# Kernel optimization log

Measured on AMD Instinct MI355X. Metric: run time of the kernel, lower is better.

## Reference

```python
import jax, jax.numpy as jnp
import numpy as np

N, D, F = 8192, 256, 64

def setup_inputs() -> dict:
    key = jax.random.key(0)
    ks = jax.random.split(key, 7)
    s = 0.02
    return {
        "x":  jax.random.normal(ks[0], (N, D), dtype=jnp.float32),
        "Wk": jax.random.normal(ks[1], (F, D), dtype=jnp.float32) * s,
        "bk": jax.random.normal(ks[2], (F,), dtype=jnp.float32) * s,
        "Wv": jax.random.normal(ks[3], (F, D), dtype=jnp.float32) * s,
        "bv": jax.random.normal(ks[4], (F,), dtype=jnp.float32) * s,
        "Wq": jax.random.normal(ks[5], (N, F, D), dtype=jnp.float32) * s,
        "bq": jax.random.normal(ks[6], (N, F), dtype=jnp.float32) * s,
    }

def reference(x, Wk, bk, Wv, bv, Wq, bq):
    # Shared K/V projections: (N, D) -> (N, F)
    k = x @ Wk.T + bk
    v = x @ Wv.T + bv
    # Per-node Q: node i uses its own weight Wq[i] on its own row x[i]
    q = jnp.einsum("nd,nfd->nf", x, Wq) + bq  # (N, F)
    # Scaled dot-product attention over nodes
    scale = 1.0 / jnp.sqrt(jnp.asarray(F, dtype=x.dtype))
    scores = (q @ k.T) * scale               # (N, N)
    attn = jax.nn.softmax(scores, axis=-1)
    return attn @ v                           # (N, F)
```

## Files before the change

### kernel.cpp

```cpp
#include <hip/hip_runtime.h>
#include <math.h>

#define NN 8192
#define DD 256
#define FF 64

typedef __attribute__((ext_vector_type(8))) __bf16 bf16x8;
typedef __attribute__((ext_vector_type(4))) __bf16 bf16x4;
typedef __attribute__((ext_vector_type(4))) float f32x4;

static __device__ __forceinline__ f32x4 mfma16(bf16x8 a, bf16x8 b, f32x4 c) {
    return __builtin_amdgcn_mfma_f32_16x16x32_bf16(a, b, c, 0, 0, 0);
}

__global__ __launch_bounds__(256) void proj_kernel(
    const float* __restrict__ x, const float* __restrict__ Wk,
    const float* __restrict__ bk, const float* __restrict__ Wv,
    const float* __restrict__ bv, const float* __restrict__ Wq,
    const float* __restrict__ bq,
    __bf16* __restrict__ q_bf, __bf16* __restrict__ k_bf,
    __bf16* __restrict__ vT)
{
    const int i = blockIdx.x;
    const int t = threadIdx.x;
    const int l = t & 63;
    const int w = t >> 6;

    const float4 xf = reinterpret_cast<const float4*>(x)[(size_t)i * 64 + l];

    const float4* wq4 = reinterpret_cast<const float4*>(Wq) + (size_t)i * 4096;
    const float4* wk4 = reinterpret_cast<const float4*>(Wk);
    const float4* wv4 = reinterpret_cast<const float4*>(Wv);

#pragma unroll
    for (int ff = 0; ff < 16; ++ff) {
        const int f = w * 16 + ff;
        float4 a = wq4[f * 64 + l];
        float s = a.x * xf.x + a.y * xf.y + a.z * xf.z + a.w * xf.w;
        s += __shfl_xor(s, 32, 64); s += __shfl_xor(s, 16, 64);
        s += __shfl_xor(s, 8, 64);  s += __shfl_xor(s, 4, 64);
        s += __shfl_xor(s, 2, 64);  s += __shfl_xor(s, 1, 64);
        if (l == 0) q_bf[(size_t)i * FF + f] = (__bf16)(s + bq[(size_t)i * FF + f]);
    }
#pragma unroll
    for (int ff = 0; ff < 16; ++ff) {
        const int f = w * 16 + ff;
        float4 a = wk4[f * 64 + l];
        float s = a.x * xf.x + a.y * xf.y + a.z * xf.z + a.w * xf.w;
        s += __shfl_xor(s, 32, 64); s += __shfl_xor(s, 16, 64);
        s += __shfl_xor(s, 8, 64);  s += __shfl_xor(s, 4, 64);
        s += __shfl_xor(s, 2, 64);  s += __shfl_xor(s, 1, 64);
        if (l == 0) k_bf[(size_t)i * FF + f] = (__bf16)(s + bk[f]);
    }
#pragma unroll
    for (int ff = 0; ff < 16; ++ff) {
        const int f = w * 16 + ff;
        float4 a = wv4[f * 64 + l];
        float s = a.x * xf.x + a.y * xf.y + a.z * xf.z + a.w * xf.w;
        s += __shfl_xor(s, 32, 64); s += __shfl_xor(s, 16, 64);
        s += __shfl_xor(s, 8, 64);  s += __shfl_xor(s, 4, 64);
        s += __shfl_xor(s, 2, 64);  s += __shfl_xor(s, 1, 64);
        if (l == 0) vT[(size_t)f * NN + i] = (__bf16)(s + bv[f]);
    }
}

__global__ __launch_bounds__(256) void attn_kernel(
    const __bf16* __restrict__ q_bf, const __bf16* __restrict__ k_bf,
    const __bf16* __restrict__ vT,
    float* __restrict__ Om, float* __restrict__ m_arr, float* __restrict__ l_arr,
    int kv_per_split)
{
    __shared__ __bf16 pT[4][16][64];

    const int lane = threadIdx.x & 63;
    const int wave = threadIdx.x >> 6;
    const int g = lane >> 4;
    const int qc = lane & 15;
    const int qb = blockIdx.x;
    const int s  = blockIdx.y;
    const int q0 = qb * 64 + wave * 16;
    const int qrow = q0 + qc;
    const float scale = 0.125f;
    const int sw = qc & 7;

    const bf16x8 qf0 = *reinterpret_cast<const bf16x8*>(q_bf + (size_t)qrow * FF + g * 8);
    const bf16x8 qf1 = *reinterpret_cast<const bf16x8*>(q_bf + (size_t)qrow * FF + 32 + g * 8);

    f32x4 o[4];
#pragma unroll
    for (int m = 0; m < 4; ++m) o[m] = (f32x4){0.f, 0.f, 0.f, 0.f};
    float mrun = -INFINITY;
    float lrun = 0.f;

    const int kv0 = s * kv_per_split;

    for (int kb = kv0; kb < kv0 + kv_per_split; kb += 64) {
        f32x4 sc[4];
#pragma unroll
        for (int kt = 0; kt < 4; ++kt) {
            const __bf16* kp = k_bf + (size_t)(kb + kt * 16 + qc) * FF + g * 8;
            bf16x8 a0 = *reinterpret_cast<const bf16x8*>(kp);
            bf16x8 a1 = *reinterpret_cast<const bf16x8*>(kp + 32);
            f32x4 acc = (f32x4){0.f, 0.f, 0.f, 0.f};
            acc = mfma16(a0, qf0, acc);
            acc = mfma16(a1, qf1, acc);
            sc[kt] = acc;
        }

        float mt = sc[0].x;
#pragma unroll
        for (int kt = 0; kt < 4; ++kt) {
            mt = fmaxf(mt, sc[kt].x); mt = fmaxf(mt, sc[kt].y);
            mt = fmaxf(mt, sc[kt].z); mt = fmaxf(mt, sc[kt].w);
        }
        mt = fmaxf(mt, __shfl_xor(mt, 16, 64));
        mt = fmaxf(mt, __shfl_xor(mt, 32, 64));
        const float mnew = fmaxf(mrun, mt * scale);
        const float alpha = __expf(mrun - mnew);

        float psum = 0.f;
#pragma unroll
        for (int kt = 0; kt < 4; ++kt) {
            float p0 = __expf(sc[kt].x * scale - mnew);
            float p1 = __expf(sc[kt].y * scale - mnew);
            float p2 = __expf(sc[kt].z * scale - mnew);
            float p3 = __expf(sc[kt].w * scale - mnew);
            psum += (p0 + p1) + (p2 + p3);
            bf16x4 pv;
            pv[0] = (__bf16)p0; pv[1] = (__bf16)p1;
            pv[2] = (__bf16)p2; pv[3] = (__bf16)p3;
            const int b = kt * 2 + (g >> 1);
            *reinterpret_cast<bf16x4*>(&pT[wave][qc][((b ^ sw) << 3) + (g & 1) * 4]) = pv;
        }
        psum += __shfl_xor(psum, 16, 64);
        psum += __shfl_xor(psum, 32, 64);
        lrun = lrun * alpha + psum;
        mrun = mnew;
#pragma unroll
        for (int m = 0; m < 4; ++m) o[m] *= alpha;

#pragma unroll
        for (int kk = 0; kk < 2; ++kk) {
            const int br = kk * 4 + g;
            bf16x8 pb = *reinterpret_cast<const bf16x8*>(&pT[wave][qc][(br ^ sw) << 3]);
            const __bf16* vp = vT + (size_t)qc * NN + kb + kk * 32 + g * 8;
#pragma unroll
            for (int m = 0; m < 4; ++m) {
                bf16x8 a = *reinterpret_cast<const bf16x8*>(vp + (size_t)m * 16 * NN);
                o[m] = mfma16(a, pb, o[m]);
            }
        }
    }

    float* op = Om + (size_t)s * FF * NN;
#pragma unroll
    for (int m = 0; m < 4; ++m) {
        op[(size_t)(m * 16 + g * 4 + 0) * NN + q0 + qc] = o[m].x;
        op[(size_t)(m * 16 + g * 4 + 1) * NN + q0 + qc] = o[m].y;
        op[(size_t)(m * 16 + g * 4 + 2) * NN + q0 + qc] = o[m].z;
        op[(size_t)(m * 16 + g * 4 + 3) * NN + q0 + qc] = o[m].w;
    }
    if (g == 0) {
        m_arr[s * NN + qrow] = mrun;
        l_arr[s * NN + qrow] = lrun;
    }
}

__global__ __launch_bounds__(256) void combine_kernel(
    const float* __restrict__ Om, const float* __restrict__ m_arr,
    const float* __restrict__ l_arr, float* __restrict__ out, int nsplit)
{
    const int idx = blockIdx.x * 256 + threadIdx.x;
    const int f = idx >> 13;
    const int i = idx & (NN - 1);

    float M = -INFINITY;
    for (int s = 0; s < nsplit; ++s) M = fmaxf(M, m_arr[s * NN + i]);
    float L = 0.f, acc = 0.f;
    for (int s = 0; s < nsplit; ++s) {
        float wgt = __expf(m_arr[s * NN + i] - M);
        L   += wgt * l_arr[s * NN + i];
        acc += wgt * Om[((size_t)s * FF + f) * NN + i];
    }
    out[(size_t)i * FF + f] = acc / L;
}

extern "C" void kernel_launch(void* const* d_in, const int* in_sizes, int n_in,
                              void* d_out, int out_size, void* d_ws, size_t ws_size,
                              hipStream_t stream) {
    const float* x  = (const float*)d_in[0];
    const float* Wk = (const float*)d_in[1];
    const float* bk = (const float*)d_in[2];
    const float* Wv = (const float*)d_in[3];
    const float* bv = (const float*)d_in[4];
    const float* Wq = (const float*)d_in[5];
    const float* bq = (const float*)d_in[6];
    float* out = (float*)d_out;

    const int nsplit = (ws_size >= (size_t)20447232) ? 8 : 4;
    const int kv_per_split = NN / nsplit;

    char* ws = (char*)d_ws;
    __bf16* q_bf = (__bf16*)(ws);
    __bf16* k_bf = (__bf16*)(ws + ((size_t)1 << 20));
    __bf16* vT   = (__bf16*)(ws + ((size_t)2 << 20));
    float*  Om   = (float*)(ws + ((size_t)3 << 20));
    float*  m_a  = (float*)(ws + ((size_t)3 << 20) + (size_t)nsplit * FF * NN * 4);
    float*  l_a  = (float*)((char*)m_a + (size_t)nsplit * NN * 4);

    hipLaunchKernelGGL(proj_kernel, dim3(NN), dim3(256), 0, stream,
                       x, Wk, bk, Wv, bv, Wq, bq, q_bf, k_bf, vT);
    hipLaunchKernelGGL(attn_kernel, dim3(NN / 64, nsplit), dim3(256), 0, stream,
                       q_bf, k_bf, vT, Om, m_a, l_a, kv_per_split);
    hipLaunchKernelGGL(combine_kernel, dim3(NN * FF / 256), dim3(256), 0, stream,
                       Om, m_a, l_a, out, nsplit);
}
```

Measured before the change: 894.7 us.

## Split projections, use MFMA for K/V, stage K/V tiles in LDS, fold scale into exp2

The single projection kernel becomes two. One computes Q with a shared-memory transpose reduction in place of per-output shuffle chains. The other computes K/V with bf16 MFMA tiles instead of scalar dot products. The attention kernel stages each 64-row K and V tile cooperatively into swizzled LDS shared by the four waves, replacing redundant per-wave global loads, and adds two barriers per iteration. The softmax scale and log2(e) are folded into Q so the kernel can use exp2 directly. K/V inputs are now rounded to bf16 before the MFMA, which lowers precision, and the workspace threshold for using 8 splits is raised.

```diff
diff --git a/kernel.cpp b/kernel.cpp
--- a/kernel.cpp
+++ b/kernel.cpp
@@ -5,6 +5,8 @@
 #define DD 256
 #define FF 64
 
+#define QSC (0.125f * 1.4426950408889634f)
+
 typedef __attribute__((ext_vector_type(8))) __bf16 bf16x8;
 typedef __attribute__((ext_vector_type(4))) __bf16 bf16x4;
 typedef __attribute__((ext_vector_type(4))) float f32x4;
@@ -13,54 +15,97 @@
     return __builtin_amdgcn_mfma_f32_16x16x32_bf16(a, b, c, 0, 0, 0);
 }
 
-__global__ __launch_bounds__(256) void proj_kernel(
-    const float* __restrict__ x, const float* __restrict__ Wk,
-    const float* __restrict__ bk, const float* __restrict__ Wv,
-    const float* __restrict__ bv, const float* __restrict__ Wq,
-    const float* __restrict__ bq,
-    __bf16* __restrict__ q_bf, __bf16* __restrict__ k_bf,
-    __bf16* __restrict__ vT)
-{
+__global__ __launch_bounds__(256) void proj_q_kernel(
+    const float* __restrict__ x, const float* __restrict__ Wq,
+    const float* __restrict__ bq, __bf16* __restrict__ q_bf)
+{
+    __shared__ float T[4][64 * 17];
+
     const int i = blockIdx.x;
-    const int t = threadIdx.x;
-    const int l = t & 63;
-    const int w = t >> 6;
+    const int l = threadIdx.x & 63;
+    const int w = threadIdx.x >> 6;
 
     const float4 xf = reinterpret_cast<const float4*>(x)[(size_t)i * 64 + l];
-
     const float4* wq4 = reinterpret_cast<const float4*>(Wq) + (size_t)i * 4096;
-    const float4* wk4 = reinterpret_cast<const float4*>(Wk);
-    const float4* wv4 = reinterpret_cast<const float4*>(Wv);
-
+
+    float pf[16];
 #pragma unroll
     for (int ff = 0; ff < 16; ++ff) {
         const int f = w * 16 + ff;
         float4 a = wq4[f * 64 + l];
-        float s = a.x * xf.x + a.y * xf.y + a.z * xf.z + a.w * xf.w;
-        s += __shfl_xor(s, 32, 64); s += __shfl_xor(s, 16, 64);
-        s += __shfl_xor(s, 8, 64);  s += __shfl_xor(s, 4, 64);
-        s += __shfl_xor(s, 2, 64);  s += __shfl_xor(s, 1, 64);
-        if (l == 0) q_bf[(size_t)i * FF + f] = (__bf16)(s + bq[(size_t)i * FF + f]);
-    }
-#pragma unroll
-    for (int ff = 0; ff < 16; ++ff) {
-        const int f = w * 16 + ff;
-        float4 a = wk4[f * 64 + l];
-        float s = a.x * xf.x + a.y * xf.y + a.z * xf.z + a.w * xf.w;
-        s += __shfl_xor(s, 32, 64); s += __shfl_xor(s, 16, 64);
-        s += __shfl_xor(s, 8, 64);  s += __shfl_xor(s, 4, 64);
-        s += __shfl_xor(s, 2, 64);  s += __shfl_xor(s, 1, 64);
-        if (l == 0) k_bf[(size_t)i * FF + f] = (__bf16)(s + bk[f]);
-    }
-#pragma unroll
-    for (int ff = 0; ff < 16; ++ff) {
-        const int f = w * 16 + ff;
-        float4 a = wv4[f * 64 + l];
-        float s = a.x * xf.x + a.y * xf.y + a.z * xf.z + a.w * xf.w;
-        s += __shfl_xor(s, 32, 64); s += __shfl_xor(s, 16, 64);
-        s += __shfl_xor(s, 8, 64);  s += __shfl_xor(s, 4, 64);
-        s += __shfl_xor(s, 2, 64);  s += __shfl_xor(s, 1, 64);
-        if (l == 0) vT[(size_t)f * NN + i] = (__bf16)(s + bv[f]);
+        pf[ff] = a.x * xf.x + a.y * xf.y + a.z * xf.z + a.w * xf.w;
+    }
+#pragma unroll
+    for (int ff = 0; ff < 16; ++ff) T[w][l * 17 + ff] = pf[ff];
+    const int f = l & 15;
+    const int c = l >> 4;
+    float s = 0.f;
+#pragma unroll
+    for (int j = 0; j < 16; ++j) s += T[w][(c * 16 + j) * 17 + f];
+    s += __shfl_xor(s, 16, 64);
+    s += __shfl_xor(s, 32, 64);
+    if (l < 16)
+        q_bf[(size_t)i * FF + w * 16 + l] =
+            (__bf16)((s + bq[(size_t)i * FF + w * 16 + l]) * QSC);
+}
+
+__global__ __launch_bounds__(256) void proj_kv_kernel(
+    const float* __restrict__ x, const float* __restrict__ Wk,
+    const float* __restrict__ bk, const float* __restrict__ Wv,
+    const float* __restrict__ bv,
+    __bf16* __restrict__ k_bf, __bf16* __restrict__ vT)
+{
+    const int lane = threadIdx.x & 63;
+    const int wave = threadIdx.x >> 6;
+    const int g = lane >> 4;
+    const int qc = lane & 15;
+    const int i0 = blockIdx.x * 64 + wave * 16;
+
+    f32x4 ack[4], acv[4];
+#pragma unroll
+    for (int nt = 0; nt < 4; ++nt) {
+        ack[nt] = (f32x4){0.f, 0.f, 0.f, 0.f};
+        acv[nt] = (f32x4){0.f, 0.f, 0.f, 0.f};
+    }
+
+    const float4* x4 = reinterpret_cast<const float4*>(x);
+#pragma unroll
+    for (int ks = 0; ks < 8; ++ks) {
+        float4 xa = x4[(size_t)(i0 + qc) * 64 + ks * 8 + g * 2];
+        float4 xb = x4[(size_t)(i0 + qc) * 64 + ks * 8 + g * 2 + 1];
+        bf16x8 af;
+        af[0] = (__bf16)xa.x; af[1] = (__bf16)xa.y; af[2] = (__bf16)xa.z; af[3] = (__bf16)xa.w;
+        af[4] = (__bf16)xb.x; af[5] = (__bf16)xb.y; af[6] = (__bf16)xb.z; af[7] = (__bf16)xb.w;
+#pragma unroll
+        for (int nt = 0; nt < 4; ++nt) {
+            const float* wkp = Wk + (size_t)(nt * 16 + qc) * DD + ks * 32 + g * 8;
+            const float* wvp = Wv + (size_t)(nt * 16 + qc) * DD + ks * 32 + g * 8;
+            float4 wa = reinterpret_cast<const float4*>(wkp)[0];
+            float4 wb = reinterpret_cast<const float4*>(wkp)[1];
+            bf16x8 bk8;
+            bk8[0] = (__bf16)wa.x; bk8[1] = (__bf16)wa.y; bk8[2] = (__bf16)wa.z; bk8[3] = (__bf16)wa.w;
+            bk8[4] = (__bf16)wb.x; bk8[5] = (__bf16)wb.y; bk8[6] = (__bf16)wb.z; bk8[7] = (__bf16)wb.w;
+            ack[nt] = mfma16(af, bk8, ack[nt]);
+            float4 va = reinterpret_cast<const float4*>(wvp)[0];
+            float4 vb = reinterpret_cast<const float4*>(wvp)[1];
+            bf16x8 bv8;
+            bv8[0] = (__bf16)va.x; bv8[1] = (__bf16)va.y; bv8[2] = (__bf16)va.z; bv8[3] = (__bf16)va.w;
+            bv8[4] = (__bf16)vb.x; bv8[5] = (__bf16)vb.y; bv8[6] = (__bf16)vb.z; bv8[7] = (__bf16)vb.w;
+            acv[nt] = mfma16(af, bv8, acv[nt]);
+        }
+    }
+
+#pragma unroll
+    for (int nt = 0; nt < 4; ++nt) {
+        const int f = nt * 16 + qc;
+        const float bkf = bk[f];
+        const float bvf = bv[f];
+#pragma unroll
+        for (int r = 0; r < 4; ++r) {
+            const int i = i0 + g * 4 + r;
+            k_bf[(size_t)i * FF + f] = (__bf16)(ack[nt][r] + bkf);
+            vT[(size_t)f * NN + i]   = (__bf16)(acv[nt][r] + bvf);
+        }
     }
 }
 
@@ -70,18 +115,22 @@
     float* __restrict__ Om, float* __restrict__ m_arr, float* __restrict__ l_arr,
     int kv_per_split)
 {
-    __shared__ __bf16 pT[4][16][64];
-
-    const int lane = threadIdx.x & 63;
-    const int wave = threadIdx.x >> 6;
+    __shared__ __align__(16) __bf16 Klds[64 * 64];
+    __shared__ __align__(16) __bf16 Vlds[64 * 64];
+    __shared__ __align__(16) __bf16 pT[4][16 * 64];
+
+    const int t = threadIdx.x;
+    const int lane = t & 63;
+    const int wave = t >> 6;
     const int g = lane >> 4;
     const int qc = lane & 15;
-    const int qb = blockIdx.x;
+    const int q0 = blockIdx.x * 64 + wave * 16;
     const int s  = blockIdx.y;
-    const int q0 = qb * 64 + wave * 16;
     const int qrow = q0 + qc;
-    const float scale = 0.125f;
     const int sw = qc & 7;
+
+    const int srow = t >> 2;
+    const int sbp  = (t & 3) * 2;
 
     const bf16x8 qf0 = *reinterpret_cast<const bf16x8*>(q_bf + (size_t)qrow * FF + g * 8);
     const bf16x8 qf1 = *reinterpret_cast<const bf16x8*>(q_bf + (size_t)qrow * FF + 32 + g * 8);
@@ -95,12 +144,27 @@
     const int kv0 = s * kv_per_split;
 
     for (int kb = kv0; kb < kv0 + kv_per_split; kb += 64) {
+        __syncthreads();
+        {
+            const __bf16* src = k_bf + (size_t)(kb + srow) * FF + sbp * 8;
+            bf16x8 u0 = *reinterpret_cast<const bf16x8*>(src);
+            bf16x8 u1 = *reinterpret_cast<const bf16x8*>(src + 8);
+            *reinterpret_cast<bf16x8*>(&Klds[srow * 64 + ((sbp ^ (srow & 7)) * 8)]) = u0;
+            *reinterpret_cast<bf16x8*>(&Klds[srow * 64 + (((sbp + 1) ^ (srow & 7)) * 8)]) = u1;
+            const __bf16* sv = vT + (size_t)srow * NN + kb + sbp * 8;
+            bf16x8 w0 = *reinterpret_cast<const bf16x8*>(sv);
+            bf16x8 w1 = *reinterpret_cast<const bf16x8*>(sv + 8);
+            *reinterpret_cast<bf16x8*>(&Vlds[srow * 64 + ((sbp ^ (srow & 7)) * 8)]) = w0;
+            *reinterpret_cast<bf16x8*>(&Vlds[srow * 64 + (((sbp + 1) ^ (srow & 7)) * 8)]) = w1;
+        }
+        __syncthreads();
+
         f32x4 sc[4];
 #pragma unroll
         for (int kt = 0; kt < 4; ++kt) {
-            const __bf16* kp = k_bf + (size_t)(kb + kt * 16 + qc) * FF + g * 8;
-            bf16x8 a0 = *reinterpret_cast<const bf16x8*>(kp);
-            bf16x8 a1 = *reinterpret_cast<const bf16x8*>(kp + 32);
+            const int row = kt * 16 + qc;
+            bf16x8 a0 = *reinterpret_cast<const bf16x8*>(&Klds[row * 64 + ((g ^ (qc & 7)) * 8)]);
+            bf16x8 a1 = *reinterpret_cast<const bf16x8*>(&Klds[row * 64 + (((4 + g) ^ (qc & 7)) * 8)]);
             f32x4 acc = (f32x4){0.f, 0.f, 0.f, 0.f};
             acc = mfma16(a0, qf0, acc);
             acc = mfma16(a1, qf1, acc);
@@ -115,22 +179,22 @@
         }
         mt = fmaxf(mt, __shfl_xor(mt, 16, 64));
         mt = fmaxf(mt, __shfl_xor(mt, 32, 64));
-        const float mnew = fmaxf(mrun, mt * scale);
-        const float alpha = __expf(mrun - mnew);
+        const float mnew = fmaxf(mrun, mt);
+        const float alpha = __builtin_amdgcn_exp2f(mrun - mnew);
 
         float psum = 0.f;
 #pragma unroll
         for (int kt = 0; kt < 4; ++kt) {
-            float p0 = __expf(sc[kt].x * scale - mnew);
-            float p1 = __expf(sc[kt].y * scale - mnew);
-            float p2 = __expf(sc[kt].z * scale - mnew);
-            float p3 = __expf(sc[kt].w * scale - mnew);
+            float p0 = __builtin_amdgcn_exp2f(sc[kt].x - mnew);
+            float p1 = __builtin_amdgcn_exp2f(sc[kt].y - mnew);
+            float p2 = __builtin_amdgcn_exp2f(sc[kt].z - mnew);
+            float p3 = __builtin_amdgcn_exp2f(sc[kt].w - mnew);
             psum += (p0 + p1) + (p2 + p3);
             bf16x4 pv;
             pv[0] = (__bf16)p0; pv[1] = (__bf16)p1;
             pv[2] = (__bf16)p2; pv[3] = (__bf16)p3;
             const int b = kt * 2 + (g >> 1);
-            *reinterpret_cast<bf16x4*>(&pT[wave][qc][((b ^ sw) << 3) + (g & 1) * 4]) = pv;
+            *reinterpret_cast<bf16x4*>(&pT[wave][qc * 64 + ((b ^ sw) << 3) + (g & 1) * 4]) = pv;
         }
         psum += __shfl_xor(psum, 16, 64);
         psum += __shfl_xor(psum, 32, 64);
@@ -142,11 +206,12 @@
 #pragma unroll
         for (int kk = 0; kk < 2; ++kk) {
             const int br = kk * 4 + g;
-            bf16x8 pb = *reinterpret_cast<const bf16x8*>(&pT[wave][qc][(br ^ sw) << 3]);
-            const __bf16* vp = vT + (size_t)qc * NN + kb + kk * 32 + g * 8;
+            bf16x8 pb = *reinterpret_cast<const bf16x8*>(&pT[wave][qc * 64 + ((br ^ sw) << 3)]);
 #pragma unroll
             for (int m = 0; m < 4; ++m) {
-                bf16x8 a = *reinterpret_cast<const bf16x8*>(vp + (size_t)m * 16 * NN);
+                const int row = m * 16 + qc;
+                bf16x8 a = *reinterpret_cast<const bf16x8*>(
+                    &Vlds[row * 64 + (((kk * 4 + g) ^ (qc & 7)) * 8)]);
                 o[m] = mfma16(a, pb, o[m]);
             }
         }
@@ -178,7 +243,7 @@
     for (int s = 0; s < nsplit; ++s) M = fmaxf(M, m_arr[s * NN + i]);
     float L = 0.f, acc = 0.f;
     for (int s = 0; s < nsplit; ++s) {
-        float wgt = __expf(m_arr[s * NN + i] - M);
+        float wgt = __builtin_amdgcn_exp2f(m_arr[s * NN + i] - M);
         L   += wgt * l_arr[s * NN + i];
         acc += wgt * Om[((size_t)s * FF + f) * NN + i];
     }
@@ -197,7 +262,7 @@
     const float* bq = (const float*)d_in[6];
     float* out = (float*)d_out;
 
-    const int nsplit = (ws_size >= (size_t)20447232) ? 8 : 4;
+    const int nsplit = (ws_size >= (size_t)20971520) ? 8 : 4;
     const int kv_per_split = NN / nsplit;
 
     char* ws = (char*)d_ws;
@@ -208,8 +273,10 @@
     float*  m_a  = (float*)(ws + ((size_t)3 << 20) + (size_t)nsplit * FF * NN * 4);
     float*  l_a  = (float*)((char*)m_a + (size_t)nsplit * NN * 4);
 
-    hipLaunchKernelGGL(proj_kernel, dim3(NN), dim3(256), 0, stream,
-                       x, Wk, bk, Wv, bv, Wq, bq, q_bf, k_bf, vT);
+    hipLaunchKernelGGL(proj_q_kernel, dim3(NN), dim3(256), 0, stream,
+                       x, Wq, bq, q_bf);
+    hipLaunchKernelGGL(proj_kv_kernel, dim3(NN / 64), dim3(256), 0, stream,
+                       x, Wk, bk, Wv, bv, k_bf, vT);
     hipLaunchKernelGGL(attn_kernel, dim3(NN / 64, nsplit), dim3(256), 0, stream,
                        q_bf, k_bf, vT, Om, m_a, l_a, kv_per_split);
     hipLaunchKernelGGL(combine_kernel, dim3(NN * FF / 256), dim3(256), 0, stream,
```

Result: faster. 766.0 us (-14.4%).
